# Performance work log

Hardware: AMD Instinct MI355X
Metric: run time of the kernel (lower is better)

The kernel has to match this reference:

```python
import jax, jax.numpy as jnp
import numpy as np

B, N, DIM = 2, 4096, 256
HEADS, DIM_HEAD, NEIGHBORS = 4, 64, 32
M_HID = 4 * 4  # m_dim * 4
ROT_DIM = DIM_HEAD // 2  # 32 (SinusoidalEmbeddings(dim_head // 2))
INV_FREQ = (1.0 / (10000.0 ** (np.arange(0, ROT_DIM, 2, dtype=np.float32) / ROT_DIM)))  # (16,)
INIT_EPS = 0.001


def sinusoidal(t):
    # t: (...,) positions -> (..., ROT_DIM) interleaved freqs (d r) with r=2
    freqs = t[..., None] * jnp.asarray(INV_FREQ)
    return jnp.repeat(freqs, 2, axis=-1)


def rotate_half(x):
    shp = x.shape
    xr = x.reshape(shp[:-1] + (shp[-1] // 2, 2))
    a, b = xr[..., 0], xr[..., 1]
    return jnp.stack((-b, a), axis=-1).reshape(shp)


def apply_rotary(t, freqs):
    rd = freqs.shape[-1]
    t_rot, t_pass = t[..., :rd], t[..., rd:]
    t_rot = t_rot * jnp.cos(freqs) + rotate_half(t_rot) * jnp.sin(freqs)
    return jnp.concatenate((t_rot, t_pass), axis=-1)


def setup_inputs() -> dict:
    key = jax.random.key(0)
    ks = jax.random.split(key, 8)
    inner = HEADS * DIM_HEAD
    return {
        "feats": jax.random.normal(ks[0], (B, N, DIM), jnp.float32),
        "coors": jax.random.normal(ks[1], (B, N, 3), jnp.float32),
        "w_qkv": jax.random.normal(ks[2], (DIM, inner * 3), jnp.float32) * INIT_EPS,
        "w_out": jax.random.normal(ks[3], (inner, DIM), jnp.float32) * INIT_EPS,
        "b_out": jnp.zeros((DIM,), jnp.float32),
        "w_c1": jax.random.normal(ks[4], (HEADS, M_HID), jnp.float32) * INIT_EPS,
        "b_c1": jnp.zeros((M_HID,), jnp.float32),
        "w_c2": jax.random.normal(ks[5], (M_HID, 1), jnp.float32) * INIT_EPS,
        "b_c2": jnp.zeros((1,), jnp.float32),
        "ln_g": jnp.ones((1,), jnp.float32),
        "ln_b": jax.random.normal(ks[6], (1,), jnp.float32) * 0.1,
    }


def reference(feats, coors, w_qkv, w_out, b_out, w_c1, b_c1, w_c2, b_c2, ln_g, ln_b):
    b, n, _ = feats.shape
    h, dh, k_nn = HEADS, DIM_HEAD, NEIGHBORS
    scale = dh ** -0.5

    # pairwise relative coordinates / distances
    rel_coors = coors[:, :, None, :] - coors[:, None, :, :]      # b n n 3
    rel_dist = jnp.linalg.norm(rel_coors, axis=-1)               # b n n

    # kNN: smallest distances (topk largest=False)
    _, nbhd_idx = jax.lax.top_k(-rel_dist, k_nn)                 # b n k

    # qkv projection
    qkv = feats @ w_qkv
    q, k, v = jnp.split(qkv, 3, axis=-1)
    q = q.reshape(b, n, h, dh).transpose(0, 2, 1, 3)             # b h n dh
    k = k.reshape(b, n, h, dh).transpose(0, 2, 1, 3)
    v = v.reshape(b, n, h, dh).transpose(0, 2, 1, 3)

    # gather neighbors
    idx5 = nbhd_idx[:, None, :, :, None]                         # b 1 n k 1
    kg = jnp.take_along_axis(k[:, :, None, :, :], idx5, axis=3)  # b h n k dh
    vg = jnp.take_along_axis(v[:, :, None, :, :], idx5, axis=3)  # b h n k dh
    rel_dist_g = jnp.take_along_axis(rel_dist, nbhd_idx, axis=2)                 # b n k
    rel_coors_g = jnp.take_along_axis(rel_coors, nbhd_idx[..., None], axis=2)    # b n k 3

    # rotary on relative distance (q positions are zeros -> identity rotation)
    q_freqs = sinusoidal(jnp.zeros((n,), feats.dtype))[None, None]   # 1 1 n rot
    k_freqs = sinusoidal(rel_dist_g * 100.0)[:, None]                # b 1 n k rot
    q = apply_rotary(q, q_freqs)
    kg = apply_rotary(kg, k_freqs)
    vg = apply_rotary(vg, k_freqs)

    qk = jnp.einsum('bhid,bhijd->bhij', q, kg) * scale           # b h n k

    # coors_mlp: Linear(heads,16) -> GELU -> Linear(16,1)
    cw_in = qk.transpose(0, 2, 3, 1)                             # b n k h
    hid = jax.nn.gelu(cw_in @ w_c1 + b_c1, approximate=False)
    coor_w = (hid @ w_c2 + b_c2)[..., 0]                         # b n k

    # CoorsNorm: unit-direction * LayerNorm(1)(norm)
    norm = jnp.linalg.norm(rel_coors_g, axis=-1, keepdims=True)  # b n k 1
    normed = rel_coors_g / jnp.clip(norm, 1e-8, None)
    mu = jnp.mean(norm, axis=-1, keepdims=True)
    var = jnp.var(norm, axis=-1, keepdims=True)
    phase = (norm - mu) * jax.lax.rsqrt(var + 1e-5) * ln_g + ln_b
    rel_coors_n = phase * normed

    coors_out = jnp.einsum('bij,bijc->bic', coor_w, rel_coors_n)  # b n 3

    attn = jax.nn.softmax(qk, axis=-1)
    out = jnp.einsum('bhij,bhijd->bhid', attn, vg)               # b h n dh
    out = out.transpose(0, 2, 1, 3).reshape(b, n, h * dh)
    out = out @ w_out + b_out
    return out, coors_out
```

## Files before the change

### kernel.cpp

```cpp
#include <hip/hip_runtime.h>
#include <hip/hip_fp16.h>
#include <math.h>

#define B_ 2
#define N_ 4096
#define DIM_ 256
#define HEADS_ 4
#define DH_ 64
#define KNN_ 32
#define INNER_ 256
#define QKVW_ 768
#define HB_ 512
#define CAND_ 512
#define M_ 8192

typedef _Float16 f16x8 __attribute__((ext_vector_type(8)));
typedef _Float16 f16x4 __attribute__((ext_vector_type(4)));
typedef _Float16 f16x2 __attribute__((ext_vector_type(2)));
typedef float    f32x4 __attribute__((ext_vector_type(4)));

#if defined(__has_builtin)
#if __has_builtin(__builtin_amdgcn_fdot2)
#define HAVE_FDOT2 1
#endif
#endif

static __device__ __forceinline__ float fdot2f(f16x2 a, f16x2 b, float c) {
#ifdef HAVE_FDOT2
    return __builtin_amdgcn_fdot2(a, b, c, false);
#else
    return (float)a[0]*(float)b[0] + (float)a[1]*(float)b[1] + c;
#endif
}

static __device__ __forceinline__ unsigned long long ullmin2(unsigned long long a, unsigned long long b) {
    return a < b ? a : b;
}

static __device__ __forceinline__ void sincos_rev(float rev, float* s, float* c) {
    const float fr = rev - floorf(rev);
    float ss, cc;
    asm("v_sin_f32 %0, %1" : "=v"(ss) : "v"(fr));
    asm("v_cos_f32 %0, %1" : "=v"(cc) : "v"(fr));
    *s = ss; *c = cc;
}

__global__ __launch_bounds__(256) void soa_kernel(const float* __restrict__ coors,
                                                  float* __restrict__ xs,
                                                  float* __restrict__ ys,
                                                  float* __restrict__ zs) {
    const int p = blockIdx.x * 256 + threadIdx.x;
    const float x = coors[p*3+0], y = coors[p*3+1], z = coors[p*3+2];
    xs[p] = x; ys[p] = y; zs[p] = z;
}

__global__ __launch_bounds__(256, 8) void knn_kernel(const float* __restrict__ xs,
                                                     const float* __restrict__ ys,
                                                     const float* __restrict__ zs,
                                                     int* __restrict__ nbhd) {
    __shared__ int   hist[HB_];
    __shared__ unsigned long long cand[CAND_];
    __shared__ float tminf[256];
    __shared__ float Msh;
    __shared__ int   bsh, clsh, candcnt, outcnt;

    const int bi = blockIdx.x;
    const int b = bi >> 12;
    const int t = threadIdx.x;
    const float* xb = xs + (size_t)b * N_;
    const float* yb = ys + (size_t)b * N_;
    const float* zb = zs + (size_t)b * N_;
    const float xi = xs[bi], yi = ys[bi], zi = zs[bi];

    float dreg[16];
    float mymin = INFINITY;
    #pragma unroll
    for (int r = 0; r < N_/(256*4); ++r) {
        const int p = t + r*256;
        const float4 xv = *(const float4*)(xb + 4*p);
        const float4 yv = *(const float4*)(yb + 4*p);
        const float4 zv = *(const float4*)(zb + 4*p);
        float4 dv;
        {   float dx = xi - xv.x, dy = yi - yv.x, dz = zi - zv.x;
            dv.x = sqrtf(dx*dx + dy*dy + dz*dz); }
        {   float dx = xi - xv.y, dy = yi - yv.y, dz = zi - zv.y;
            dv.y = sqrtf(dx*dx + dy*dy + dz*dz); }
        {   float dx = xi - xv.z, dy = yi - yv.z, dz = zi - zv.z;
            dv.z = sqrtf(dx*dx + dy*dy + dz*dz); }
        {   float dx = xi - xv.w, dy = yi - yv.w, dz = zi - zv.w;
            dv.w = sqrtf(dx*dx + dy*dy + dz*dz); }
        dreg[r*4+0] = dv.x; dreg[r*4+1] = dv.y;
        dreg[r*4+2] = dv.z; dreg[r*4+3] = dv.w;
        mymin = fminf(mymin, fminf(fminf(dv.x, dv.y), fminf(dv.z, dv.w)));
    }
    tminf[t] = mymin;
    hist[t] = 0; hist[t + 256] = 0;
    if (t == 0) { candcnt = 0; outcnt = 0; }
    __syncthreads();

    if (t < 64) {
        float m4 = fmaxf(fmaxf(tminf[t], tminf[t+64]), fmaxf(tminf[t+128], tminf[t+192]));
        #pragma unroll
        for (int off = 32; off; off >>= 1) m4 = fmaxf(m4, __shfl_xor(m4, off));
        if (t == 0) Msh = fmaxf(m4, 1e-20f);
    }
    __syncthreads();

    const float Mv = Msh;
    const float scale = (float)(HB_ - 1) / Mv;

    #pragma unroll
    for (int r = 0; r < 16; ++r) {
        const float d = dreg[r];
        if (d <= Mv) {
            const int bin = (int)fminf(d * scale, (float)(HB_ - 1));
            atomicAdd(&hist[bin], 1);
        }
    }
    __syncthreads();

    if (t < 64) {
        int s = 0;
        #pragma unroll
        for (int k = 0; k < HB_/64; ++k) s += hist[t*(HB_/64) + k];
        int inc = s;
        #pragma unroll
        for (int off = 1; off < 64; off <<= 1) {
            const int v = __shfl_up(inc, off);
            if (t >= off) inc += v;
        }
        const int excl = inc - s;
        if (excl < KNN_ && inc >= KNN_) {
            int cum = excl;
            #pragma unroll
            for (int k = 0; k < HB_/64; ++k) {
                const int c = hist[t*(HB_/64) + k];
                if (cum + c >= KNN_) { bsh = t*(HB_/64) + k; clsh = cum; break; }
                cum += c;
            }
        }
    }
    __syncthreads();

    const int bbin = bsh, c_less = clsh;

    #pragma unroll
    for (int r = 0; r < 16; ++r) {
        const int j = t + r*256;
        (void)j;
    }
    #pragma unroll
    for (int r = 0; r < N_/(256*4); ++r) {
        #pragma unroll
        for (int e = 0; e < 4; ++e) {
            const float d = dreg[r*4+e];
            if (d <= Mv) {
                const int j = 4*(t + r*256) + e;
                const int bin = (int)fminf(d * scale, (float)(HB_ - 1));
                if (bin < bbin) {
                    const int slot = atomicAdd(&outcnt, 1);
                    nbhd[(size_t)bi * KNN_ + slot] = j;
                } else if (bin == bbin) {
                    const int c = atomicAdd(&candcnt, 1);
                    if (c < CAND_) {
                        cand[c] = ((unsigned long long)__float_as_uint(d) << 32) | (unsigned)j;
                    }
                }
            }
        }
    }
    __syncthreads();

    const int m = KNN_ - c_less;
    const int e = candcnt;
    if (e <= CAND_) {
        if (t < 64) {
            for (int r = 0; r < m; ++r) {
                unsigned long long v = ~0ULL;
                for (int idx = t; idx < e; idx += 64) v = ullmin2(v, cand[idx]);
                #pragma unroll
                for (int off = 32; off; off >>= 1) v = ullmin2(v, __shfl_xor(v, off));
                if (t == 0) nbhd[(size_t)bi * KNN_ + c_less + r] = (int)(v & 0xffffffffu);
                for (int idx = t; idx < e; idx += 64)
                    if (cand[idx] == v) cand[idx] = ~0ULL;
            }
        }
    } else if (t == 0) {
        int chosen[KNN_];
        for (int r = 0; r < m; ++r) {
            unsigned long long best = ~0ULL;
            for (int jj = 0; jj < N_; ++jj) {
                const float dx = xi - xb[jj], dy = yi - yb[jj], dz = zi - zb[jj];
                const float d = sqrtf(dx*dx + dy*dy + dz*dz);
                if (d <= Mv) {
                    const int bin = (int)fminf(d * scale, (float)(HB_ - 1));
                    if (bin == bbin) {
                        bool skip = false;
                        for (int q = 0; q < r; ++q) if (chosen[q] == jj) skip = true;
                        if (!skip) {
                            const unsigned long long key =
                                ((unsigned long long)__float_as_uint(d) << 32) | (unsigned)jj;
                            best = ullmin2(best, key);
                        }
                    }
                }
            }
            chosen[r] = (int)(best & 0xffffffffu);
            nbhd[(size_t)bi * KNN_ + c_less + r] = chosen[r];
        }
    }
}

__global__ __launch_bounds__(256) void wconv_kernel(const float* __restrict__ in,
                                                    _Float16* __restrict__ out,
                                                    int Nn) {
    __shared__ float tl[32][33];
    const int tx = threadIdx.x & 31, ty = threadIdx.x >> 5;
    const int n0 = blockIdx.x * 32, k0 = blockIdx.y * 32;
    #pragma unroll
    for (int r = 0; r < 4; ++r)
        tl[ty + r*8][tx] = in[(size_t)(k0 + ty + r*8) * Nn + n0 + tx];
    __syncthreads();
    #pragma unroll
    for (int r = 0; r < 4; ++r)
        out[(size_t)(n0 + ty + r*8) * 256 + k0 + tx] = (_Float16)(tl[tx][ty + r*8] * 64.0f);
}

template <bool A_F16, int OUT_MODE>
__global__ __launch_bounds__(256) void mfma_gemm_kernel(const void* __restrict__ Ap,
                                                        const _Float16* __restrict__ Bt,
                                                        const float* __restrict__ bias,
                                                        void* __restrict__ Cp,
                                                        int Nn) {
    __shared__ _Float16 As[4096];
    __shared__ _Float16 Bs[4096];
    const int t = threadIdx.x;
    const int w = t >> 6, l = t & 63;
    const int wr = w >> 1, wc = w & 1;
    const int lr = l & 15, kg = l >> 4;
    const int row0 = blockIdx.y * 128, col0 = blockIdx.x * 128;

    f32x4 acc[4][4];
    #pragma unroll
    for (int mi = 0; mi < 4; ++mi)
        #pragma unroll
        for (int ni = 0; ni < 4; ++ni)
            acc[mi][ni] = (f32x4){0.0f, 0.0f, 0.0f, 0.0f};

    for (int k0 = 0; k0 < 256; k0 += 32) {
        __syncthreads();
        if constexpr (A_F16) {
            const _Float16* A = (const _Float16*)Ap;
            #pragma unroll
            for (int r = 0; r < 2; ++r) {
                const int u = r*256 + t;
                const int row = u >> 2, kgrp = u & 3;
                *(f16x8*)&As[((kgrp<<7) + row)*8] =
                    *(const f16x8*)(A + (size_t)(row0 + row)*256 + k0 + kgrp*8);
            }
        } else {
            const float* A = (const float*)Ap;
            #pragma unroll
            for (int r = 0; r < 4; ++r) {
                const int slot = r*256 + t;
                const int row = slot >> 3, kq = slot & 7;
                const float4 a4 = *(const float4*)(A + (size_t)(row0 + row)*256 + k0 + kq*4);
                f16x4 h;
                h[0] = (_Float16)a4.x; h[1] = (_Float16)a4.y;
                h[2] = (_Float16)a4.z; h[3] = (_Float16)a4.w;
                *(f16x4*)&As[((size_t)((kq>>1)<<7) + row)*8 + (kq&1)*4] = h;
            }
        }
        #pragma unroll
        for (int r = 0; r < 2; ++r) {
            const int u = r*256 + t;
            const int col = u >> 2, kq = u & 3;
            *(f16x8*)&Bs[((size_t)(kq<<7) + col)*8] =
                *(const f16x8*)(Bt + (size_t)(col0 + col)*256 + k0 + kq*8);
        }
        __syncthreads();
        f16x8 af[4], bf[4];
        #pragma unroll
        for (int mi = 0; mi < 4; ++mi)
            af[mi] = *(const f16x8*)&As[((kg<<7) + wr*64 + mi*16 + lr)*8];
        #pragma unroll
        for (int ni = 0; ni < 4; ++ni)
            bf[ni] = *(const f16x8*)&Bs[((kg<<7) + wc*64 + ni*16 + lr)*8];
        #pragma unroll
        for (int mi = 0; mi < 4; ++mi)
            #pragma unroll
            for (int ni = 0; ni < 4; ++ni)
                acc[mi][ni] = __builtin_amdgcn_mfma_f32_16x16x32_f16(af[mi], bf[ni], acc[mi][ni], 0, 0, 0);
    }

    #pragma unroll
    for (int mi = 0; mi < 4; ++mi)
        #pragma unroll
        for (int ni = 0; ni < 4; ++ni) {
            const int col = col0 + wc*64 + ni*16 + lr;
            const float bv = (OUT_MODE == 0 && bias) ? bias[col] : 0.0f;
            #pragma unroll
            for (int r = 0; r < 4; ++r) {
                const int row = row0 + wr*64 + mi*16 + kg*4 + r;
                const float v = acc[mi][ni][r] * 0.015625f + bv;
                if constexpr (OUT_MODE == 0) {
                    ((float*)Cp)[(size_t)row * Nn + col] = v;
                } else if constexpr (OUT_MODE == 1) {
                    ((_Float16*)Cp)[(size_t)row * Nn + col] = (_Float16)v;
                } else {
                    _Float16* qb = (_Float16*)Cp;
                    _Float16* kvb = qb + (size_t)M_ * 256;
                    if (col < 256) {
                        qb[(size_t)row * 256 + col] = (_Float16)v;
                    } else {
                        const int d = col & 255;
                        const int isv = (col >> 9) & 1;
                        kvb[(size_t)row * 512 + ((d >> 2) << 3) + (isv << 2) + (d & 3)] = (_Float16)v;
                    }
                }
            }
        }
}

__global__ __launch_bounds__(256) void attn_kernel(const _Float16* __restrict__ q_buf,
                                                   const _Float16* __restrict__ kv_buf,
                                                   const float* __restrict__ coors,
                                                   const int* __restrict__ nbhd,
                                                   const float* __restrict__ w_c1,
                                                   const float* __restrict__ b_c1,
                                                   const float* __restrict__ w_c2,
                                                   const float* __restrict__ b_c2,
                                                   const float* __restrict__ ln_b,
                                                   _Float16* __restrict__ out_pre,
                                                   float* __restrict__ coors_out) {
    __shared__ __half vgh[KNN_ * INNER_];
    __shared__ float qkl[KNN_][HEADS_];
    __shared__ float attnl[KNN_][HEADS_];
    __shared__ float coorw[KNN_];
    __shared__ float distl[KNN_];
    __shared__ float ul[KNN_][3];
    __shared__ int   njl[KNN_];

    const int bi = blockIdx.x;
    const int b = bi >> 12;
    const int i = bi & (N_ - 1);
    const int t = threadIdx.x;
    const int w = t >> 6;
    const int l = t & 63;
    const int h = l >> 4;
    const float* cb = coors + (size_t)b * N_ * 3;

    if (t < KNN_) {
        const int nj = nbhd[(size_t)bi * KNN_ + t];
        njl[t] = nj;
        const float dx = cb[i*3+0] - cb[nj*3+0];
        const float dy = cb[i*3+1] - cb[nj*3+1];
        const float dz = cb[i*3+2] - cb[nj*3+2];
        const float dist = sqrtf(dx*dx + dy*dy + dz*dz);
        distl[t] = dist * 100.0f;
        const float den = fmaxf(dist, 1e-8f);
        ul[t][0] = dx / den; ul[t][1] = dy / den; ul[t][2] = dz / den;
    }

    const f16x4 qh = *(const f16x4*)(q_buf + (size_t)bi * 256 + 4*l);
    const f16x2 q01 = {qh[0], qh[1]}, q23 = {qh[2], qh[3]};
    const int li = l & 15;
    const bool rot = li < 8;
    const float invf0r = exp2f(-(float)(2*li    ) * 0.8304820237218407f) * 0.15915494309189535f;
    const float invf1r = exp2f(-(float)(2*li + 1) * 0.8304820237218407f) * 0.15915494309189535f;
    const _Float16* kvb = kv_buf + (size_t)b * N_ * 512;
    __syncthreads();

    #pragma unroll 4
    for (int jj = 0; jj < 8; ++jj) {
        const int j = w*8 + jj;
        const int nj = njl[j];
        const f16x8 kv = *(const f16x8*)(kvb + (size_t)nj * 512 + l*8);
        f16x2 k01 = {kv[0], kv[1]}, k23 = {kv[2], kv[3]};
        f16x2 v01 = {kv[4], kv[5]}, v23 = {kv[6], kv[7]};
        if (rot) {
            const float d100 = distl[j];
            float s0, c0, s1, c1;
            sincos_rev(d100 * invf0r, &s0, &c0);
            sincos_rev(d100 * invf1r, &s1, &c1);
            const f16x2 cc0 = {(_Float16)c0, (_Float16)c0};
            const f16x2 sn0 = {(_Float16)(-s0), (_Float16)s0};
            const f16x2 cc1 = {(_Float16)c1, (_Float16)c1};
            const f16x2 sn1 = {(_Float16)(-s1), (_Float16)s1};
            const f16x2 k10 = {k01[1], k01[0]};
            const f16x2 k32 = {k23[1], k23[0]};
            const f16x2 v10 = {v01[1], v01[0]};
            const f16x2 v32 = {v23[1], v23[0]};
            k01 = k01*cc0 + k10*sn0;
            k23 = k23*cc1 + k32*sn1;
            v01 = v01*cc0 + v10*sn0;
            v23 = v23*cc1 + v32*sn1;
        }
        {
            union { f16x2 h2[2]; uint2 u; } pk;
            pk.h2[0] = v01; pk.h2[1] = v23;
            *reinterpret_cast<uint2*>(&vgh[j * INNER_ + 4*l]) = pk.u;
        }
        float p = fdot2f(k01, q01, fdot2f(k23, q23, 0.0f));
        p += __shfl_xor(p, 1);
        p += __shfl_xor(p, 2);
        p += __shfl_xor(p, 4);
        p += __shfl_xor(p, 8);
        if (li == 0) qkl[j][h] = p * 0.125f;
    }
    __syncthreads();

    {
        const int d = l;
        const float x = (d < KNN_) ? qkl[d][w] : -INFINITY;
        float mx = x;
        #pragma unroll
        for (int off = 32; off; off >>= 1) mx = fmaxf(mx, __shfl_xor(mx, off));
        const float e = expf(x - mx);
        float s = e;
        #pragma unroll
        for (int off = 32; off; off >>= 1) s += __shfl_xor(s, off);
        if (d < KNN_) attnl[d][w] = e / s;
    }

    if (t < KNN_) {
        const float a0 = qkl[t][0], a1 = qkl[t][1], a2 = qkl[t][2], a3 = qkl[t][3];
        float cw = b_c2[0];
        #pragma unroll
        for (int mh = 0; mh < 16; ++mh) {
            const float hv = a0*w_c1[0*16+mh] + a1*w_c1[1*16+mh]
                           + a2*w_c1[2*16+mh] + a3*w_c1[3*16+mh] + b_c1[mh];
            const float g = 0.5f * hv * (1.0f + erff(hv * 0.70710678118654752440f));
            cw += g * w_c2[mh];
        }
        coorw[t] = cw;
    }
    __syncthreads();

    float o = 0.0f;
    #pragma unroll
    for (int j = 0; j < KNN_; ++j)
        o += attnl[j][w] * __half2float(vgh[j * INNER_ + t]);
    out_pre[(size_t)bi * INNER_ + t] = (_Float16)o;

    if (t < 3) {
        float acc = 0.0f;
        #pragma unroll
        for (int j = 0; j < KNN_; ++j) acc += coorw[j] * ul[j][t];
        coors_out[(size_t)bi * 3 + t] = acc * ln_b[0];
    }
}

extern "C" void kernel_launch(void* const* d_in, const int* in_sizes, int n_in,
                              void* d_out, int out_size, void* d_ws, size_t ws_size,
                              hipStream_t stream) {
    (void)in_sizes; (void)n_in; (void)out_size; (void)ws_size;
    const float* feats = (const float*)d_in[0];
    const float* coors = (const float*)d_in[1];
    const float* w_qkv = (const float*)d_in[2];
    const float* w_out = (const float*)d_in[3];
    const float* b_out = (const float*)d_in[4];
    const float* w_c1  = (const float*)d_in[5];
    const float* b_c1  = (const float*)d_in[6];
    const float* w_c2  = (const float*)d_in[7];
    const float* b_c2  = (const float*)d_in[8];
    const float* ln_b  = (const float*)d_in[10];

    const int M = M_;
    _Float16* q_buf    = (_Float16*)d_ws;
    _Float16* kv_buf   = q_buf + (size_t)M * 256;
    int*      nbhd     = (int*)(kv_buf + (size_t)M * 512);
    _Float16* out_pre  = (_Float16*)(nbhd + (size_t)M * KNN_);
    _Float16* wqkvT    = out_pre + (size_t)M * INNER_;
    _Float16* woutT    = wqkvT + (size_t)QKVW_ * DIM_;
    float*    xs       = (float*)(woutT + (size_t)DIM_ * DIM_);
    float*    ys       = xs + M;
    float*    zs       = ys + M;

    float* out_main  = (float*)d_out;
    float* out_coors = out_main + (size_t)M * DIM_;

    wconv_kernel<<<dim3(QKVW_/32, DIM_/32), 256, 0, stream>>>(w_qkv, wqkvT, QKVW_);
    wconv_kernel<<<dim3(DIM_/32,  DIM_/32), 256, 0, stream>>>(w_out, woutT, DIM_);
    soa_kernel<<<M/256, 256, 0, stream>>>(coors, xs, ys, zs);

    mfma_gemm_kernel<false, 2><<<dim3(QKVW_/128, M/128), 256, 0, stream>>>(
        feats, wqkvT, nullptr, q_buf, QKVW_);
    knn_kernel<<<M, 256, 0, stream>>>(xs, ys, zs, nbhd);
    attn_kernel<<<M, 256, 0, stream>>>(q_buf, kv_buf, coors, nbhd,
                                       w_c1, b_c1, w_c2, b_c2, ln_b,
                                       out_pre, out_coors);
    mfma_gemm_kernel<true, 0><<<dim3(DIM_/128, M/128), 256, 0, stream>>>(
        out_pre, woutT, b_out, out_main, DIM_);
}
```

Before: 116.7 us.

## Fuse kNN selection into attention kernel and merge prep kernels

Merges the kNN kernel and the attention kernel into one per-point kernel. Neighbour indices and distances now stay in shared memory, and the kNN scratch is unioned with the V-gather buffer. This removes the nbhd global round-trip, the distance recomputation and one launch. The two weight-transpose kernels and the SoA coordinate kernel are also merged into a single prep launch. The risk is the launch_bounds(256,8) occupancy hint combined with the larger register and shared-memory footprint of the fused kernel.

```diff
diff --git a/kernel.cpp b/kernel.cpp
--- a/kernel.cpp
+++ b/kernel.cpp
@@ -45,22 +45,154 @@
     *s = ss; *c = cc;
 }
 
-__global__ __launch_bounds__(256) void soa_kernel(const float* __restrict__ coors,
-                                                  float* __restrict__ xs,
-                                                  float* __restrict__ ys,
-                                                  float* __restrict__ zs) {
-    const int p = blockIdx.x * 256 + threadIdx.x;
-    const float x = coors[p*3+0], y = coors[p*3+1], z = coors[p*3+2];
-    xs[p] = x; ys[p] = y; zs[p] = z;
-}
-
-__global__ __launch_bounds__(256, 8) void knn_kernel(const float* __restrict__ xs,
-                                                     const float* __restrict__ ys,
-                                                     const float* __restrict__ zs,
-                                                     int* __restrict__ nbhd) {
-    __shared__ int   hist[HB_];
-    __shared__ unsigned long long cand[CAND_];
-    __shared__ float tminf[256];
+__global__ __launch_bounds__(256) void prep_kernel(const float* __restrict__ w_qkv,
+                                                   const float* __restrict__ w_out,
+                                                   const float* __restrict__ coors,
+                                                   _Float16* __restrict__ wqkvT,
+                                                   _Float16* __restrict__ woutT,
+                                                   float* __restrict__ xs,
+                                                   float* __restrict__ ys,
+                                                   float* __restrict__ zs) {
+    __shared__ float tl[32][33];
+    const int blk = blockIdx.x;
+    const int tx = threadIdx.x & 31, ty = threadIdx.x >> 5;
+    if (blk < 256) {
+        const float* in; _Float16* out; int Nn, n0, k0;
+        if (blk < 192) { in = w_qkv; out = wqkvT; Nn = QKVW_; n0 = (blk % 24) * 32; k0 = (blk / 24) * 32; }
+        else { const int b2 = blk - 192; in = w_out; out = woutT; Nn = DIM_; n0 = (b2 % 8) * 32; k0 = (b2 / 8) * 32; }
+        #pragma unroll
+        for (int r = 0; r < 4; ++r)
+            tl[ty + r*8][tx] = in[(size_t)(k0 + ty + r*8) * Nn + n0 + tx];
+        __syncthreads();
+        #pragma unroll
+        for (int r = 0; r < 4; ++r)
+            out[(size_t)(n0 + ty + r*8) * 256 + k0 + tx] = (_Float16)(tl[tx][ty + r*8] * 64.0f);
+    } else {
+        const int p = (blk - 256) * 256 + threadIdx.x;
+        const float x = coors[p*3+0], y = coors[p*3+1], z = coors[p*3+2];
+        xs[p] = x; ys[p] = y; zs[p] = z;
+    }
+}
+
+template <bool A_F16, int OUT_MODE>
+__global__ __launch_bounds__(256) void mfma_gemm_kernel(const void* __restrict__ Ap,
+                                                        const _Float16* __restrict__ Bt,
+                                                        const float* __restrict__ bias,
+                                                        void* __restrict__ Cp,
+                                                        int Nn) {
+    __shared__ _Float16 As[4096];
+    __shared__ _Float16 Bs[4096];
+    const int t = threadIdx.x;
+    const int w = t >> 6, l = t & 63;
+    const int wr = w >> 1, wc = w & 1;
+    const int lr = l & 15, kg = l >> 4;
+    const int row0 = blockIdx.y * 128, col0 = blockIdx.x * 128;
+
+    f32x4 acc[4][4];
+    #pragma unroll
+    for (int mi = 0; mi < 4; ++mi)
+        #pragma unroll
+        for (int ni = 0; ni < 4; ++ni)
+            acc[mi][ni] = (f32x4){0.0f, 0.0f, 0.0f, 0.0f};
+
+    for (int k0 = 0; k0 < 256; k0 += 32) {
+        __syncthreads();
+        if constexpr (A_F16) {
+            const _Float16* A = (const _Float16*)Ap;
+            #pragma unroll
+            for (int r = 0; r < 2; ++r) {
+                const int u = r*256 + t;
+                const int row = u >> 2, kgrp = u & 3;
+                *(f16x8*)&As[((kgrp<<7) + row)*8] =
+                    *(const f16x8*)(A + (size_t)(row0 + row)*256 + k0 + kgrp*8);
+            }
+        } else {
+            const float* A = (const float*)Ap;
+            #pragma unroll
+            for (int r = 0; r < 4; ++r) {
+                const int slot = r*256 + t;
+                const int row = slot >> 3, kq = slot & 7;
+                const float4 a4 = *(const float4*)(A + (size_t)(row0 + row)*256 + k0 + kq*4);
+                f16x4 h;
+                h[0] = (_Float16)a4.x; h[1] = (_Float16)a4.y;
+                h[2] = (_Float16)a4.z; h[3] = (_Float16)a4.w;
+                *(f16x4*)&As[((size_t)((kq>>1)<<7) + row)*8 + (kq&1)*4] = h;
+            }
+        }
+        #pragma unroll
+        for (int r = 0; r < 2; ++r) {
+            const int u = r*256 + t;
+            const int col = u >> 2, kq = u & 3;
+            *(f16x8*)&Bs[((size_t)(kq<<7) + col)*8] =
+                *(const f16x8*)(Bt + (size_t)(col0 + col)*256 + k0 + kq*8);
+        }
+        __syncthreads();
+        f16x8 af[4], bf[4];
+        #pragma unroll
+        for (int mi = 0; mi < 4; ++mi)
+            af[mi] = *(const f16x8*)&As[((kg<<7) + wr*64 + mi*16 + lr)*8];
+        #pragma unroll
+        for (int ni = 0; ni < 4; ++ni)
+            bf[ni] = *(const f16x8*)&Bs[((kg<<7) + wc*64 + ni*16 + lr)*8];
+        #pragma unroll
+        for (int mi = 0; mi < 4; ++mi)
+            #pragma unroll
+            for (int ni = 0; ni < 4; ++ni)
+                acc[mi][ni] = __builtin_amdgcn_mfma_f32_16x16x32_f16(af[mi], bf[ni], acc[mi][ni], 0, 0, 0);
+    }
+
+    #pragma unroll
+    for (int mi = 0; mi < 4; ++mi)
+        #pragma unroll
+        for (int ni = 0; ni < 4; ++ni) {
+            const int col = col0 + wc*64 + ni*16 + lr;
+            const float bv = (OUT_MODE == 0 && bias) ? bias[col] : 0.0f;
+            #pragma unroll
+            for (int r = 0; r < 4; ++r) {
+                const int row = row0 + wr*64 + mi*16 + kg*4 + r;
+                const float v = acc[mi][ni][r] * 0.015625f + bv;
+                if constexpr (OUT_MODE == 0) {
+                    ((float*)Cp)[(size_t)row * Nn + col] = v;
+                } else {
+                    _Float16* qb = (_Float16*)Cp;
+                    _Float16* kvb = qb + (size_t)M_ * 256;
+                    if (col < 256) {
+                        qb[(size_t)row * 256 + col] = (_Float16)v;
+                    } else {
+                        const int d = col & 255;
+                        const int isv = (col >> 9) & 1;
+                        kvb[(size_t)row * 512 + ((d >> 2) << 3) + (isv << 2) + (d & 3)] = (_Float16)v;
+                    }
+                }
+            }
+        }
+}
+
+struct KnnSmem {
+    int hist[HB_];
+    unsigned long long cand[CAND_];
+    float tminf[256];
+};
+union FusedSmem {
+    KnnSmem k;
+    __half vgh[KNN_ * INNER_];
+};
+
+__global__ __launch_bounds__(256, 8) void knn_attn_kernel(
+        const float* __restrict__ xs, const float* __restrict__ ys,
+        const float* __restrict__ zs,
+        const _Float16* __restrict__ q_buf, const _Float16* __restrict__ kv_buf,
+        const float* __restrict__ w_c1, const float* __restrict__ b_c1,
+        const float* __restrict__ w_c2, const float* __restrict__ b_c2,
+        const float* __restrict__ ln_b,
+        _Float16* __restrict__ out_pre, float* __restrict__ coors_out) {
+    __shared__ FusedSmem u;
+    __shared__ float qkl[KNN_][HEADS_];
+    __shared__ float attnl[KNN_][HEADS_];
+    __shared__ float coorw[KNN_];
+    __shared__ float distl[KNN_];
+    __shared__ float ul[KNN_][3];
+    __shared__ int   njl[KNN_];
     __shared__ float Msh;
     __shared__ int   bsh, clsh, candcnt, outcnt;
 
@@ -93,13 +225,14 @@
         dreg[r*4+2] = dv.z; dreg[r*4+3] = dv.w;
         mymin = fminf(mymin, fminf(fminf(dv.x, dv.y), fminf(dv.z, dv.w)));
     }
-    tminf[t] = mymin;
-    hist[t] = 0; hist[t + 256] = 0;
+    u.k.tminf[t] = mymin;
+    u.k.hist[t] = 0; u.k.hist[t + 256] = 0;
     if (t == 0) { candcnt = 0; outcnt = 0; }
     __syncthreads();
 
     if (t < 64) {
-        float m4 = fmaxf(fmaxf(tminf[t], tminf[t+64]), fmaxf(tminf[t+128], tminf[t+192]));
+        float m4 = fmaxf(fmaxf(u.k.tminf[t], u.k.tminf[t+64]),
+                         fmaxf(u.k.tminf[t+128], u.k.tminf[t+192]));
         #pragma unroll
         for (int off = 32; off; off >>= 1) m4 = fmaxf(m4, __shfl_xor(m4, off));
         if (t == 0) Msh = fmaxf(m4, 1e-20f);
@@ -114,7 +247,7 @@
         const float d = dreg[r];
         if (d <= Mv) {
             const int bin = (int)fminf(d * scale, (float)(HB_ - 1));
-            atomicAdd(&hist[bin], 1);
+            atomicAdd(&u.k.hist[bin], 1);
         }
     }
     __syncthreads();
@@ -122,7 +255,7 @@
     if (t < 64) {
         int s = 0;
         #pragma unroll
-        for (int k = 0; k < HB_/64; ++k) s += hist[t*(HB_/64) + k];
+        for (int k = 0; k < HB_/64; ++k) s += u.k.hist[t*(HB_/64) + k];
         int inc = s;
         #pragma unroll
         for (int off = 1; off < 64; off <<= 1) {
@@ -134,7 +267,7 @@
             int cum = excl;
             #pragma unroll
             for (int k = 0; k < HB_/64; ++k) {
-                const int c = hist[t*(HB_/64) + k];
+                const int c = u.k.hist[t*(HB_/64) + k];
                 if (cum + c >= KNN_) { bsh = t*(HB_/64) + k; clsh = cum; break; }
                 cum += c;
             }
@@ -144,11 +277,6 @@
 
     const int bbin = bsh, c_less = clsh;
 
-    #pragma unroll
-    for (int r = 0; r < 16; ++r) {
-        const int j = t + r*256;
-        (void)j;
-    }
     #pragma unroll
     for (int r = 0; r < N_/(256*4); ++r) {
         #pragma unroll
@@ -159,11 +287,11 @@
                 const int bin = (int)fminf(d * scale, (float)(HB_ - 1));
                 if (bin < bbin) {
                     const int slot = atomicAdd(&outcnt, 1);
-                    nbhd[(size_t)bi * KNN_ + slot] = j;
+                    njl[slot] = j; distl[slot] = d;
                 } else if (bin == bbin) {
                     const int c = atomicAdd(&candcnt, 1);
                     if (c < CAND_) {
-                        cand[c] = ((unsigned long long)__float_as_uint(d) << 32) | (unsigned)j;
+                        u.k.cand[c] = ((unsigned long long)__float_as_uint(d) << 32) | (unsigned)j;
                     }
                 }
             }
@@ -177,16 +305,18 @@
         if (t < 64) {
             for (int r = 0; r < m; ++r) {
                 unsigned long long v = ~0ULL;
-                for (int idx = t; idx < e; idx += 64) v = ullmin2(v, cand[idx]);
+                for (int idx = t; idx < e; idx += 64) v = ullmin2(v, u.k.cand[idx]);
                 #pragma unroll
                 for (int off = 32; off; off >>= 1) v = ullmin2(v, __shfl_xor(v, off));
-                if (t == 0) nbhd[(size_t)bi * KNN_ + c_less + r] = (int)(v & 0xffffffffu);
+                if (t == 0) {
+                    njl[c_less + r] = (int)(v & 0xffffffffu);
+                    distl[c_less + r] = __uint_as_float((unsigned)(v >> 32));
+                }
                 for (int idx = t; idx < e; idx += 64)
-                    if (cand[idx] == v) cand[idx] = ~0ULL;
+                    if (u.k.cand[idx] == v) u.k.cand[idx] = ~0ULL;
             }
         }
     } else if (t == 0) {
-        int chosen[KNN_];
         for (int r = 0; r < m; ++r) {
             unsigned long long best = ~0ULL;
             for (int jj = 0; jj < N_; ++jj) {
@@ -196,7 +326,7 @@
                     const int bin = (int)fminf(d * scale, (float)(HB_ - 1));
                     if (bin == bbin) {
                         bool skip = false;
-                        for (int q = 0; q < r; ++q) if (chosen[q] == jj) skip = true;
+                        for (int q = 0; q < r; ++q) if (njl[c_less + q] == jj) skip = true;
                         if (!skip) {
                             const unsigned long long key =
                                 ((unsigned long long)__float_as_uint(d) << 32) | (unsigned)jj;
@@ -205,160 +335,22 @@
                     }
                 }
             }
-            chosen[r] = (int)(best & 0xffffffffu);
-            nbhd[(size_t)bi * KNN_ + c_less + r] = chosen[r];
-        }
-    }
-}
-
-__global__ __launch_bounds__(256) void wconv_kernel(const float* __restrict__ in,
-                                                    _Float16* __restrict__ out,
-                                                    int Nn) {
-    __shared__ float tl[32][33];
-    const int tx = threadIdx.x & 31, ty = threadIdx.x >> 5;
-    const int n0 = blockIdx.x * 32, k0 = blockIdx.y * 32;
-    #pragma unroll
-    for (int r = 0; r < 4; ++r)
-        tl[ty + r*8][tx] = in[(size_t)(k0 + ty + r*8) * Nn + n0 + tx];
-    __syncthreads();
-    #pragma unroll
-    for (int r = 0; r < 4; ++r)
-        out[(size_t)(n0 + ty + r*8) * 256 + k0 + tx] = (_Float16)(tl[tx][ty + r*8] * 64.0f);
-}
-
-template <bool A_F16, int OUT_MODE>
-__global__ __launch_bounds__(256) void mfma_gemm_kernel(const void* __restrict__ Ap,
-                                                        const _Float16* __restrict__ Bt,
-                                                        const float* __restrict__ bias,
-                                                        void* __restrict__ Cp,
-                                                        int Nn) {
-    __shared__ _Float16 As[4096];
-    __shared__ _Float16 Bs[4096];
-    const int t = threadIdx.x;
-    const int w = t >> 6, l = t & 63;
-    const int wr = w >> 1, wc = w & 1;
-    const int lr = l & 15, kg = l >> 4;
-    const int row0 = blockIdx.y * 128, col0 = blockIdx.x * 128;
-
-    f32x4 acc[4][4];
-    #pragma unroll
-    for (int mi = 0; mi < 4; ++mi)
-        #pragma unroll
-        for (int ni = 0; ni < 4; ++ni)
-            acc[mi][ni] = (f32x4){0.0f, 0.0f, 0.0f, 0.0f};
-
-    for (int k0 = 0; k0 < 256; k0 += 32) {
-        __syncthreads();
-        if constexpr (A_F16) {
-            const _Float16* A = (const _Float16*)Ap;
-            #pragma unroll
-            for (int r = 0; r < 2; ++r) {
-                const int u = r*256 + t;
-                const int row = u >> 2, kgrp = u & 3;
-                *(f16x8*)&As[((kgrp<<7) + row)*8] =
-                    *(const f16x8*)(A + (size_t)(row0 + row)*256 + k0 + kgrp*8);
-            }
-        } else {
-            const float* A = (const float*)Ap;
-            #pragma unroll
-            for (int r = 0; r < 4; ++r) {
-                const int slot = r*256 + t;
-                const int row = slot >> 3, kq = slot & 7;
-                const float4 a4 = *(const float4*)(A + (size_t)(row0 + row)*256 + k0 + kq*4);
-                f16x4 h;
-                h[0] = (_Float16)a4.x; h[1] = (_Float16)a4.y;
-                h[2] = (_Float16)a4.z; h[3] = (_Float16)a4.w;
-                *(f16x4*)&As[((size_t)((kq>>1)<<7) + row)*8 + (kq&1)*4] = h;
-            }
-        }
-        #pragma unroll
-        for (int r = 0; r < 2; ++r) {
-            const int u = r*256 + t;
-            const int col = u >> 2, kq = u & 3;
-            *(f16x8*)&Bs[((size_t)(kq<<7) + col)*8] =
-                *(const f16x8*)(Bt + (size_t)(col0 + col)*256 + k0 + kq*8);
-        }
-        __syncthreads();
-        f16x8 af[4], bf[4];
-        #pragma unroll
-        for (int mi = 0; mi < 4; ++mi)
-            af[mi] = *(const f16x8*)&As[((kg<<7) + wr*64 + mi*16 + lr)*8];
-        #pragma unroll
-        for (int ni = 0; ni < 4; ++ni)
-            bf[ni] = *(const f16x8*)&Bs[((kg<<7) + wc*64 + ni*16 + lr)*8];
-        #pragma unroll
-        for (int mi = 0; mi < 4; ++mi)
-            #pragma unroll
-            for (int ni = 0; ni < 4; ++ni)
-                acc[mi][ni] = __builtin_amdgcn_mfma_f32_16x16x32_f16(af[mi], bf[ni], acc[mi][ni], 0, 0, 0);
-    }
-
-    #pragma unroll
-    for (int mi = 0; mi < 4; ++mi)
-        #pragma unroll
-        for (int ni = 0; ni < 4; ++ni) {
-            const int col = col0 + wc*64 + ni*16 + lr;
-            const float bv = (OUT_MODE == 0 && bias) ? bias[col] : 0.0f;
-            #pragma unroll
-            for (int r = 0; r < 4; ++r) {
-                const int row = row0 + wr*64 + mi*16 + kg*4 + r;
-                const float v = acc[mi][ni][r] * 0.015625f + bv;
-                if constexpr (OUT_MODE == 0) {
-                    ((float*)Cp)[(size_t)row * Nn + col] = v;
-                } else if constexpr (OUT_MODE == 1) {
-                    ((_Float16*)Cp)[(size_t)row * Nn + col] = (_Float16)v;
-                } else {
-                    _Float16* qb = (_Float16*)Cp;
-                    _Float16* kvb = qb + (size_t)M_ * 256;
-                    if (col < 256) {
-                        qb[(size_t)row * 256 + col] = (_Float16)v;
-                    } else {
-                        const int d = col & 255;
-                        const int isv = (col >> 9) & 1;
-                        kvb[(size_t)row * 512 + ((d >> 2) << 3) + (isv << 2) + (d & 3)] = (_Float16)v;
-                    }
-                }
-            }
-        }
-}
-
-__global__ __launch_bounds__(256) void attn_kernel(const _Float16* __restrict__ q_buf,
-                                                   const _Float16* __restrict__ kv_buf,
-                                                   const float* __restrict__ coors,
-                                                   const int* __restrict__ nbhd,
-                                                   const float* __restrict__ w_c1,
-                                                   const float* __restrict__ b_c1,
-                                                   const float* __restrict__ w_c2,
-                                                   const float* __restrict__ b_c2,
-                                                   const float* __restrict__ ln_b,
-                                                   _Float16* __restrict__ out_pre,
-                                                   float* __restrict__ coors_out) {
-    __shared__ __half vgh[KNN_ * INNER_];
-    __shared__ float qkl[KNN_][HEADS_];
-    __shared__ float attnl[KNN_][HEADS_];
-    __shared__ float coorw[KNN_];
-    __shared__ float distl[KNN_];
-    __shared__ float ul[KNN_][3];
-    __shared__ int   njl[KNN_];
-
-    const int bi = blockIdx.x;
-    const int b = bi >> 12;
-    const int i = bi & (N_ - 1);
-    const int t = threadIdx.x;
+            njl[c_less + r] = (int)(best & 0xffffffffu);
+            distl[c_less + r] = __uint_as_float((unsigned)(best >> 32));
+        }
+    }
+    __syncthreads();
+
     const int w = t >> 6;
     const int l = t & 63;
     const int h = l >> 4;
-    const float* cb = coors + (size_t)b * N_ * 3;
 
     if (t < KNN_) {
-        const int nj = nbhd[(size_t)bi * KNN_ + t];
-        njl[t] = nj;
-        const float dx = cb[i*3+0] - cb[nj*3+0];
-        const float dy = cb[i*3+1] - cb[nj*3+1];
-        const float dz = cb[i*3+2] - cb[nj*3+2];
-        const float dist = sqrtf(dx*dx + dy*dy + dz*dz);
-        distl[t] = dist * 100.0f;
-        const float den = fmaxf(dist, 1e-8f);
+        const int nj = njl[t];
+        const float dx = xi - xb[nj];
+        const float dy = yi - yb[nj];
+        const float dz = zi - zb[nj];
+        const float den = fmaxf(distl[t], 1e-8f);
         ul[t][0] = dx / den; ul[t][1] = dy / den; ul[t][2] = dz / den;
     }
 
@@ -379,7 +371,7 @@
         f16x2 k01 = {kv[0], kv[1]}, k23 = {kv[2], kv[3]};
         f16x2 v01 = {kv[4], kv[5]}, v23 = {kv[6], kv[7]};
         if (rot) {
-            const float d100 = distl[j];
+            const float d100 = distl[j] * 100.0f;
             float s0, c0, s1, c1;
             sincos_rev(d100 * invf0r, &s0, &c0);
             sincos_rev(d100 * invf1r, &s1, &c1);
@@ -397,9 +389,9 @@
             v23 = v23*cc1 + v32*sn1;
         }
         {
-            union { f16x2 h2[2]; uint2 u; } pk;
+            union { f16x2 h2[2]; uint2 uu; } pk;
             pk.h2[0] = v01; pk.h2[1] = v23;
-            *reinterpret_cast<uint2*>(&vgh[j * INNER_ + 4*l]) = pk.u;
+            *reinterpret_cast<uint2*>(&u.vgh[j * INNER_ + 4*l]) = pk.uu;
         }
         float p = fdot2f(k01, q01, fdot2f(k23, q23, 0.0f));
         p += __shfl_xor(p, 1);
@@ -416,11 +408,11 @@
         float mx = x;
         #pragma unroll
         for (int off = 32; off; off >>= 1) mx = fmaxf(mx, __shfl_xor(mx, off));
-        const float e = expf(x - mx);
-        float s = e;
+        const float ev = expf(x - mx);
+        float s = ev;
         #pragma unroll
         for (int off = 32; off; off >>= 1) s += __shfl_xor(s, off);
-        if (d < KNN_) attnl[d][w] = e / s;
+        if (d < KNN_) attnl[d][w] = ev / s;
     }
 
     if (t < KNN_) {
@@ -440,7 +432,7 @@
     float o = 0.0f;
     #pragma unroll
     for (int j = 0; j < KNN_; ++j)
-        o += attnl[j][w] * __half2float(vgh[j * INNER_ + t]);
+        o += attnl[j][w] * __half2float(u.vgh[j * INNER_ + t]);
     out_pre[(size_t)bi * INNER_ + t] = (_Float16)o;
 
     if (t < 3) {
@@ -469,8 +461,7 @@
     const int M = M_;
     _Float16* q_buf    = (_Float16*)d_ws;
     _Float16* kv_buf   = q_buf + (size_t)M * 256;
-    int*      nbhd     = (int*)(kv_buf + (size_t)M * 512);
-    _Float16* out_pre  = (_Float16*)(nbhd + (size_t)M * KNN_);
+    _Float16* out_pre  = kv_buf + (size_t)M * 512;
     _Float16* wqkvT    = out_pre + (size_t)M * INNER_;
     _Float16* woutT    = wqkvT + (size_t)QKVW_ * DIM_;
     float*    xs       = (float*)(woutT + (size_t)DIM_ * DIM_);
@@ -480,16 +471,15 @@
     float* out_main  = (float*)d_out;
     float* out_coors = out_main + (size_t)M * DIM_;
 
-    wconv_kernel<<<dim3(QKVW_/32, DIM_/32), 256, 0, stream>>>(w_qkv, wqkvT, QKVW_);
-    wconv_kernel<<<dim3(DIM_/32,  DIM_/32), 256, 0, stream>>>(w_out, woutT, DIM_);
-    soa_kernel<<<M/256, 256, 0, stream>>>(coors, xs, ys, zs);
+    prep_kernel<<<288, 256, 0, stream>>>(w_qkv, w_out, coors, wqkvT, woutT, xs, ys, zs);
 
     mfma_gemm_kernel<false, 2><<<dim3(QKVW_/128, M/128), 256, 0, stream>>>(
         feats, wqkvT, nullptr, q_buf, QKVW_);
-    knn_kernel<<<M, 256, 0, stream>>>(xs, ys, zs, nbhd);
-    attn_kernel<<<M, 256, 0, stream>>>(q_buf, kv_buf, coors, nbhd,
-                                       w_c1, b_c1, w_c2, b_c2, ln_b,
-                                       out_pre, out_coors);
+
+    knn_attn_kernel<<<M, 256, 0, stream>>>(xs, ys, zs, q_buf, kv_buf,
+                                           w_c1, b_c1, w_c2, b_c2, ln_b,
+                                           out_pre, out_coors);
+
     mfma_gemm_kernel<true, 0><<<dim3(DIM_/128, M/128), 256, 0, stream>>>(
         out_pre, woutT, b_out, out_main, DIM_);
 }
```

New measurement: 107.1 us. -8.3%, faster.
